# Kernel tuning notes

Measured on AMD Instinct MI355X. Metric: run time of the kernel, lower is better.

Reference implementation:

```python
import jax, jax.numpy as jnp
import numpy as np

B, T, I, H = 32, 512, 128, 512


def setup_inputs() -> dict:
    key = jax.random.key(0)
    ks = jax.random.split(key, 9)
    sH = 1.0 / np.sqrt(H)
    sI = 1.0 / np.sqrt(I)
    return {
        "values": jax.random.normal(ks[0], (B, T, I), jnp.float32),
        "Deltas": jax.random.uniform(ks[1], (B, T, 1), jnp.float32),
        "ys": jax.random.normal(ks[2], (B, T, 1), jnp.float32),
        # LSTMCell params (torch gate order: i, f, g, o)
        "W_ih": jax.random.uniform(ks[3], (4 * H, I), jnp.float32, -sH, sH),
        "W_hh": jax.random.uniform(ks[4], (4 * H, H), jnp.float32, -sH, sH),
        "b_ih": jax.random.uniform(ks[5], (4 * H,), jnp.float32, -sH, sH),
        "b_hh": jax.random.uniform(ks[6], (4 * H,), jnp.float32, -sH, sH),
        # atten_linear: input_size -> input_size
        "atten_W": jax.random.uniform(ks[7], (I, I), jnp.float32, -sI, sI),
        "atten_b": jax.random.uniform(ks[8], (I,), jnp.float32, -sI, sI),
    }


def lstm_cell(x, h, c, W_ih, W_hh, b_ih, b_hh):
    gates = x @ W_ih.T + b_ih + h @ W_hh.T + b_hh
    i, f, g, o = jnp.split(gates, 4, axis=-1)
    c_new = jax.nn.sigmoid(f) * c + jax.nn.sigmoid(i) * jnp.tanh(g)
    h_new = jax.nn.sigmoid(o) * jnp.tanh(c_new)
    return h_new, c_new


def reference(values, Deltas, ys, W_ih, W_hh, b_ih, b_hh, atten_W, atten_b):
    Bs, Ts, Is = values.shape
    Hs = W_hh.shape[1]
    dt = values.dtype
    # cumulative time gaps and pairwise decay matrix D[b,t,j] = cum[t] - cum[j]
    dcum = jnp.cumsum(Deltas, axis=-2)[..., 0]          # [B,T]
    D = dcum[:, :, None] - dcum[:, None, :]             # [B,T,T]
    # attention scores: linear(values) @ original_values^T
    v = values @ atten_W.T + atten_b                    # [B,T,I]
    a_tj = jnp.einsum('bti,bsi->bts', v, values)        # [B,T,T]
    # t = 0 step with zero initial state
    h0 = jnp.zeros((Bs, Hs), dt)
    c0 = jnp.zeros((Bs, Hs), dt)
    h, c = lstm_cell(v[:, 0], h0, c0, W_ih, W_hh, b_ih, b_hh)
    c_n = jnp.zeros((Bs, Ts, Hs), dt).at[:, 0].set(c)
    idx = jnp.arange(Ts)
    NEG = jnp.finfo(dt).min
    e = jnp.asarray(np.e, dt)

    def step(carry, t):
        h, c_n = carry
        mask = idx < t                                   # causal window j < t
        logits = jnp.where(mask, a_tj[:, t], NEG)
        alpha = jax.nn.softmax(logits, axis=-1)          # masked entries ~0
        w = jnp.where(mask, 1.0 / jnp.log(e + D[:, t]), 0.0)
        alpha = alpha * w
        C = jnp.einsum('bj,bjh->bh', alpha, c_n)         # weighted cell history
        h_new, c_new = lstm_cell(v[:, t], h, C, W_ih, W_hh, b_ih, b_hh)
        return (h_new, c_n.at[:, t].set(c_new)), h_new

    (_, _), hs = jax.lax.scan(step, (h, c_n), jnp.arange(1, Ts))
    h_n = jnp.concatenate([h[:, None], jnp.swapaxes(hs, 0, 1)], axis=1)
    return h_n
```

## Files before the change

kernel.cpp:

```cpp
#include <hip/hip_runtime.h>
#include <math.h>

#define B_  32
#define T_  512
#define I_  128
#define H_  512
#define G4_ 2048
#define GB_ 64
#define NG_ 4

__global__ __launch_bounds__(256) void gemm_abt(
    const float* __restrict__ A, const float* __restrict__ Bm, float* __restrict__ C,
    const float* __restrict__ bias, long sA, long sB, long sC, int ldc)
{
  __shared__ float Al[64][65];
  __shared__ float Bl[64][65];
  const long z = blockIdx.z;
  A += z * sA; Bm += z * sB; C += z * sC;
  const int m0 = blockIdx.x * 64, n0 = blockIdx.y * 64;
  const int tid = threadIdx.x;
  const int tx = tid & 15, ty = tid >> 4;
  float acc[4][4] = {};

  for (int h = 0; h < 2; ++h) {
    const int k0 = h * 64;
    __syncthreads();
    #pragma unroll
    for (int s = 0; s < 4; ++s) {
      int idx = tid + s * 256;
      int m  = idx >> 4;
      int k4 = (idx & 15) << 2;
      float4 a4 = *(const float4*)&A[(long)(m0 + m) * 128 + k0 + k4];
      Al[k4 + 0][m] = a4.x; Al[k4 + 1][m] = a4.y; Al[k4 + 2][m] = a4.z; Al[k4 + 3][m] = a4.w;
      float4 b4 = *(const float4*)&Bm[(long)(n0 + m) * 128 + k0 + k4];
      Bl[k4 + 0][m] = b4.x; Bl[k4 + 1][m] = b4.y; Bl[k4 + 2][m] = b4.z; Bl[k4 + 3][m] = b4.w;
    }
    __syncthreads();
    #pragma unroll 8
    for (int k = 0; k < 64; ++k) {
      float a0 = Al[k][ty*4+0], a1 = Al[k][ty*4+1], a2 = Al[k][ty*4+2], a3 = Al[k][ty*4+3];
      float b0 = Bl[k][tx*4+0], b1 = Bl[k][tx*4+1], b2 = Bl[k][tx*4+2], b3 = Bl[k][tx*4+3];
      acc[0][0] += a0*b0; acc[0][1] += a0*b1; acc[0][2] += a0*b2; acc[0][3] += a0*b3;
      acc[1][0] += a1*b0; acc[1][1] += a1*b1; acc[1][2] += a1*b2; acc[1][3] += a1*b3;
      acc[2][0] += a2*b0; acc[2][1] += a2*b1; acc[2][2] += a2*b2; acc[2][3] += a2*b3;
      acc[3][0] += a3*b0; acc[3][1] += a3*b1; acc[3][2] += a3*b2; acc[3][3] += a3*b3;
    }
  }
  #pragma unroll
  for (int i = 0; i < 4; ++i) {
    #pragma unroll
    for (int j = 0; j < 4; ++j) {
      float bb = bias ? bias[n0 + tx*4 + j] : 0.f;
      C[(long)(m0 + ty*4 + i) * ldc + n0 + tx*4 + j] = acc[i][j] + bb;
    }
  }
}

__global__ __launch_bounds__(512) void cumsum_k(const float* __restrict__ Deltas,
                                                float* __restrict__ dcum)
{
  __shared__ float s[512];
  const int b = blockIdx.x, t = threadIdx.x;
  s[t] = Deltas[b * 512 + t];
  __syncthreads();
  for (int off = 1; off < 512; off <<= 1) {
    float v = (t >= off) ? s[t - off] : 0.f;
    __syncthreads();
    s[t] += v;
    __syncthreads();
  }
  dcum[b * 512 + t] = s[t];
}

__global__ __launch_bounds__(64) void softmax_k(float* __restrict__ a,
                                                const float* __restrict__ dcum)
{
  const int t = blockIdx.x, b = blockIdx.y;
  float* row = a + ((long)b * T_ + t) * T_;
  const int lane = threadIdx.x;
  if (t == 0) {
    #pragma unroll
    for (int i = 0; i < 8; ++i) row[i * 64 + lane] = 0.f;
    return;
  }
  float vals[8];
  float mx = -3.4e38f;
  #pragma unroll
  for (int i = 0; i < 8; ++i) {
    int j = i * 64 + lane;
    float v = (j < t) ? row[j] : -3.4e38f;
    vals[i] = v; mx = fmaxf(mx, v);
  }
  #pragma unroll
  for (int off = 1; off < 64; off <<= 1) mx = fmaxf(mx, __shfl_xor(mx, off));
  float sum = 0.f;
  #pragma unroll
  for (int i = 0; i < 8; ++i) {
    int j = i * 64 + lane;
    float e = (j < t) ? expf(vals[i] - mx) : 0.f;
    vals[i] = e; sum += e;
  }
  #pragma unroll
  for (int off = 1; off < 64; off <<= 1) sum += __shfl_xor(sum, off);
  const float E = 2.718281828459045f;
  const float dct = dcum[b * 512 + t];
  const float inv = 1.f / sum;
  #pragma unroll
  for (int i = 0; i < 8; ++i) {
    int j = i * 64 + lane;
    float w = (j < t) ? 1.f / logf(E + dct - dcum[b * 512 + j]) : 0.f;
    row[j] = vals[i] * inv * w;
  }
}

__device__ __forceinline__ void st_wt(float* p, float v) {
  __hip_atomic_store(p, v, __ATOMIC_RELAXED, __HIP_MEMORY_SCOPE_AGENT);
}
__device__ __forceinline__ float ld_wt(const float* p) {
  return __hip_atomic_load(p, __ATOMIC_RELAXED, __HIP_MEMORY_SCOPE_AGENT);
}

__device__ __forceinline__ void bar_arrive(unsigned* cnt, unsigned* gen) {
  unsigned old = __hip_atomic_fetch_add(cnt, 1u, __ATOMIC_RELAXED, __HIP_MEMORY_SCOPE_AGENT);
  if (old == GB_ - 1u) {
    __hip_atomic_store(cnt, 0u, __ATOMIC_RELAXED, __HIP_MEMORY_SCOPE_AGENT);
    asm volatile("s_waitcnt vmcnt(0)" ::: "memory");
    __hip_atomic_fetch_add(gen, 1u, __ATOMIC_RELAXED, __HIP_MEMORY_SCOPE_AGENT);
  }
}
__device__ __forceinline__ int bar_wait(unsigned* gen, unsigned target, unsigned* abrt) {
  long spins = 0;
  for (;;) {
    unsigned g = __hip_atomic_load(gen, __ATOMIC_RELAXED, __HIP_MEMORY_SCOPE_AGENT);
    if ((int)(g - target) >= 0) return 0;
    if (((++spins) & 255) == 0) {
      if (__hip_atomic_load(abrt, __ATOMIC_RELAXED, __HIP_MEMORY_SCOPE_AGENT)) return 1;
      if (spins > 6000000L) {
        __hip_atomic_store(abrt, 1u, __ATOMIC_RELAXED, __HIP_MEMORY_SCOPE_AGENT);
        return 1;
      }
    }
    __builtin_amdgcn_s_sleep(1);
  }
}

__global__ __launch_bounds__(256, 1) void recurrent_k(
    const float* __restrict__ v_buf,
    const float* __restrict__ alpha,
    const float* __restrict__ W_ih,
    const float* __restrict__ W_hh,
    const float* __restrict__ b_ih, const float* __restrict__ b_hh,
    float* gates,
    float* out,
    unsigned* bar)
{
  extern __shared__ float lds[];
  float* hv  = lds;
  float* cn  = lds + 8 * 640;
  float* red = cn + 512 * 64;
  __shared__ int s_ab;

  const int tid = threadIdx.x;
  const int g = blockIdx.x;
  const int grp = g >> 6;
  const int rs = g & 63, bg = grp;
  const int b_u = g >> 3, hs = g & 7;
  const int r_l = tid >> 3, cg = tid & 7;
  const int row = rs * 32 + r_l;
  const int jg = tid >> 6, l = tid & 63;

  unsigned* cntA = bar + grp * 128 + 0;
  unsigned* genA = bar + grp * 128 + 32;
  unsigned* cntB = bar + grp * 128 + 64;
  unsigned* genB = bar + grp * 128 + 96;
  unsigned* abrt = bar + 1023;

  float4 wreg[20];
  #pragma unroll
  for (int k = 0; k < 20; ++k) {
    int c0 = cg * 4 + k * 32;
    if (k < 4) wreg[k] = *(const float4*)&W_ih[(long)row * I_ + c0];
    else       wreg[k] = *(const float4*)&W_hh[(long)row * H_ + (c0 - 128)];
  }
  const float bias = b_ih[row] + b_hh[row];

  for (int t = 0; t < T_; ++t) {
    if (tid == 0) s_ab = bar_wait(genA, (unsigned)t, abrt);
    __syncthreads();
    if (s_ab) return;

    {
      int bp = tid >> 5, c4 = (tid & 31) << 2;
      float4 vv = *(const float4*)&v_buf[((long)(bg * 8 + bp) * T_ + t) * I_ + c4];
      *(float4*)&hv[bp * 640 + c4] = vv;
    }
    if (t > 0) {
      #pragma unroll
      for (int s = 0; s < 16; ++s) {
        int idx = tid + s * 256;
        int bp = idx >> 9, c = idx & 511;
        hv[bp * 640 + 128 + c] = ld_wt(&out[((long)(bg * 8 + bp) * T_ + (t - 1)) * H_ + c]);
      }
    } else {
      #pragma unroll
      for (int s = 0; s < 16; ++s) {
        int idx = tid + s * 256;
        int bp = idx >> 9, c = idx & 511;
        hv[bp * 640 + 128 + c] = 0.f;
      }
    }
    __syncthreads();

    float acc[8] = {};
    #pragma unroll
    for (int k = 0; k < 20; ++k) {
      float4 w4 = wreg[k];
      #pragma unroll
      for (int bp = 0; bp < 8; ++bp) {
        float4 x = *(const float4*)&hv[bp * 640 + cg * 4 + k * 32];
        acc[bp] += w4.x * x.x + w4.y * x.y + w4.z * x.z + w4.w * x.w;
      }
    }
    #pragma unroll
    for (int off = 1; off < 8; off <<= 1) {
      #pragma unroll
      for (int bp = 0; bp < 8; ++bp) acc[bp] += __shfl_xor(acc[bp], off);
    }
    if (cg == 0) {
      #pragma unroll
      for (int bp = 0; bp < 8; ++bp)
        st_wt(&gates[(long)(bg * 8 + bp) * G4_ + row], acc[bp] + bias);
    }
    __syncthreads();
    if (tid == 0) bar_arrive(cntB, genB);

    float partial = 0.f;
    {
      const float* arow = alpha + ((long)b_u * T_ + t) * T_;
      int j0 = jg * 128, j1 = j0 + 128; if (j1 > t) j1 = t;
      for (int j = j0; j < j1; ++j)
        partial += arow[j] * cn[j * 64 + l];
    }
    red[tid] = partial;
    if (tid == 0) s_ab = bar_wait(genB, (unsigned)(t + 1), abrt);
    __syncthreads();
    if (s_ab) return;

    if (tid < 64) {
      const long gb = (long)b_u * G4_ + hs * 64 + l;
      float gi = ld_wt(&gates[gb]);
      float gf = ld_wt(&gates[gb + H_]);
      float gg = ld_wt(&gates[gb + 2 * H_]);
      float go = ld_wt(&gates[gb + 3 * H_]);
      float C  = red[l] + red[64 + l] + red[128 + l] + red[192 + l];
      float si = 1.f / (1.f + expf(-gi));
      float sf = 1.f / (1.f + expf(-gf));
      float so = 1.f / (1.f + expf(-go));
      float cnew = sf * C + si * tanhf(gg);
      float hnew = so * tanhf(cnew);
      st_wt(&out[((long)b_u * T_ + t) * H_ + hs * 64 + l], hnew);
      cn[t * 64 + l] = cnew;
    }
    __syncthreads();
    if (tid == 0) bar_arrive(cntA, genA);
  }
}

extern "C" void kernel_launch(void* const* d_in, const int* in_sizes, int n_in,
                              void* d_out, int out_size, void* d_ws, size_t ws_size,
                              hipStream_t stream)
{
  const float* values  = (const float*)d_in[0];
  const float* Deltas  = (const float*)d_in[1];
  const float* W_ih    = (const float*)d_in[3];
  const float* W_hh    = (const float*)d_in[4];
  const float* b_ih    = (const float*)d_in[5];
  const float* b_hh    = (const float*)d_in[6];
  const float* atten_W = (const float*)d_in[7];
  const float* atten_b = (const float*)d_in[8];
  float* out = (float*)d_out;

  char* ws = (char*)d_ws;
  unsigned* bar = (unsigned*)ws;
  float* v_buf  = (float*)(ws + 4096);
  float* a_buf  = (float*)(ws + 4096 + 8388608);
  float* dcum   = (float*)(ws + 4096 + 8388608 + 33554432);
  float* gates  = (float*)(ws + 4096 + 8388608 + 33554432 + 65536);

  hipMemsetAsync(bar, 0, 4096, stream);

  gemm_abt<<<dim3(256, 2, 1), 256, 0, stream>>>(values, atten_W, v_buf, atten_b,
                                                0, 0, 0, 128);
  cumsum_k<<<32, 512, 0, stream>>>(Deltas, dcum);
  gemm_abt<<<dim3(8, 8, 32), 256, 0, stream>>>(v_buf, values, a_buf, nullptr,
                                               512L * 128, 512L * 128, 512L * 512, 512);
  softmax_k<<<dim3(512, 32), 64, 0, stream>>>(a_buf, dcum);

  (void)hipFuncSetAttribute((const void*)recurrent_k,
                            hipFuncAttributeMaxDynamicSharedMemorySize, 152576);
  recurrent_k<<<256, 256, 152576, stream>>>(v_buf, a_buf, W_ih, W_hh, b_ih, b_hh,
                                            gates, out, bar);
}
```

Before: 16.60 ms.

## Replace counter barriers with per-block flags and precompute input projection off critical path

Swaps the atomic counter plus generation grid barrier for per-block monotonic flags. Each block publishes its step, and 64 lanes poll one group's flags together with a wave-wide all-check. This removes the serialized atomic increment chain from each barrier. The W_ih·v input projection for the next step is now computed while waiting on the second barrier, so it leaves the critical path, and the t=0 hidden-state zero-fill is skipped. The risks are more polling traffic and a lower spin timeout.

```diff
diff --git a/kernel.cpp b/kernel.cpp
--- a/kernel.cpp
+++ b/kernel.cpp
@@ -7,7 +7,6 @@
 #define H_  512
 #define G4_ 2048
 #define GB_ 64
-#define NG_ 4
 
 __global__ __launch_bounds__(256) void gemm_abt(
     const float* __restrict__ A, const float* __restrict__ Bm, float* __restrict__ C,
@@ -119,23 +118,19 @@
 __device__ __forceinline__ float ld_wt(const float* p) {
   return __hip_atomic_load(p, __ATOMIC_RELAXED, __HIP_MEMORY_SCOPE_AGENT);
 }
-
-__device__ __forceinline__ void bar_arrive(unsigned* cnt, unsigned* gen) {
-  unsigned old = __hip_atomic_fetch_add(cnt, 1u, __ATOMIC_RELAXED, __HIP_MEMORY_SCOPE_AGENT);
-  if (old == GB_ - 1u) {
-    __hip_atomic_store(cnt, 0u, __ATOMIC_RELAXED, __HIP_MEMORY_SCOPE_AGENT);
-    asm volatile("s_waitcnt vmcnt(0)" ::: "memory");
-    __hip_atomic_fetch_add(gen, 1u, __ATOMIC_RELAXED, __HIP_MEMORY_SCOPE_AGENT);
-  }
-}
-__device__ __forceinline__ int bar_wait(unsigned* gen, unsigned target, unsigned* abrt) {
+__device__ __forceinline__ void flag_set(unsigned* f, unsigned v) {
+  __hip_atomic_store(f, v, __ATOMIC_RELAXED, __HIP_MEMORY_SCOPE_AGENT);
+}
+__device__ __forceinline__ int poll64(const unsigned* flags, unsigned target,
+                                      unsigned* abrt) {
   long spins = 0;
   for (;;) {
-    unsigned g = __hip_atomic_load(gen, __ATOMIC_RELAXED, __HIP_MEMORY_SCOPE_AGENT);
-    if ((int)(g - target) >= 0) return 0;
-    if (((++spins) & 255) == 0) {
+    unsigned f = __hip_atomic_load(&flags[threadIdx.x], __ATOMIC_RELAXED,
+                                   __HIP_MEMORY_SCOPE_AGENT);
+    if (__all((int)(f >= target))) return 0;
+    if (((++spins) & 63) == 0) {
       if (__hip_atomic_load(abrt, __ATOMIC_RELAXED, __HIP_MEMORY_SCOPE_AGENT)) return 1;
-      if (spins > 6000000L) {
+      if (spins > 1500000L) {
         __hip_atomic_store(abrt, 1u, __ATOMIC_RELAXED, __HIP_MEMORY_SCOPE_AGENT);
         return 1;
       }
@@ -156,69 +151,75 @@
 {
   extern __shared__ float lds[];
   float* hv  = lds;
-  float* cn  = lds + 8 * 640;
+  float* cn  = lds + 8 * 512;
   float* red = cn + 512 * 64;
   __shared__ int s_ab;
 
   const int tid = threadIdx.x;
   const int g = blockIdx.x;
   const int grp = g >> 6;
-  const int rs = g & 63, bg = grp;
+  const int bg = grp;
+  const int rs = g & 63;
   const int b_u = g >> 3, hs = g & 7;
   const int r_l = tid >> 3, cg = tid & 7;
   const int row = rs * 32 + r_l;
   const int jg = tid >> 6, l = tid & 63;
 
-  unsigned* cntA = bar + grp * 128 + 0;
-  unsigned* genA = bar + grp * 128 + 32;
-  unsigned* cntB = bar + grp * 128 + 64;
-  unsigned* genB = bar + grp * 128 + 96;
-  unsigned* abrt = bar + 1023;
-
-  float4 wreg[20];
-  #pragma unroll
-  for (int k = 0; k < 20; ++k) {
-    int c0 = cg * 4 + k * 32;
-    if (k < 4) wreg[k] = *(const float4*)&W_ih[(long)row * I_ + c0];
-    else       wreg[k] = *(const float4*)&W_hh[(long)row * H_ + (c0 - 128)];
-  }
+  unsigned* flagA = bar;
+  unsigned* flagB = bar + 256;
+  unsigned* abrt  = bar + 512;
+  const unsigned* fA = flagA + grp * 64;
+  const unsigned* fB = flagB + grp * 64;
+
+  float4 wh[16];
+  #pragma unroll
+  for (int k = 0; k < 16; ++k)
+    wh[k] = *(const float4*)&W_hh[(long)row * H_ + cg * 4 + k * 32];
+  float4 wv[4];
+  #pragma unroll
+  for (int k = 0; k < 4; ++k)
+    wv[k] = *(const float4*)&W_ih[(long)row * I_ + cg * 4 + k * 32];
   const float bias = b_ih[row] + b_hh[row];
 
+  float vacc[8];
+  #pragma unroll
+  for (int bp = 0; bp < 8; ++bp) {
+    float a = 0.f;
+    #pragma unroll
+    for (int k = 0; k < 4; ++k) {
+      float4 x = *(const float4*)&v_buf[((long)(bg * 8 + bp) * T_) * I_ + cg * 4 + k * 32];
+      a += wv[k].x * x.x + wv[k].y * x.y + wv[k].z * x.z + wv[k].w * x.w;
+    }
+    vacc[bp] = a;
+  }
+
   for (int t = 0; t < T_; ++t) {
-    if (tid == 0) s_ab = bar_wait(genA, (unsigned)t, abrt);
+    if (tid < 64) { int ab = poll64(fA, (unsigned)t, abrt); if (tid == 0) s_ab = ab; }
     __syncthreads();
     if (s_ab) return;
 
-    {
-      int bp = tid >> 5, c4 = (tid & 31) << 2;
-      float4 vv = *(const float4*)&v_buf[((long)(bg * 8 + bp) * T_ + t) * I_ + c4];
-      *(float4*)&hv[bp * 640 + c4] = vv;
-    }
     if (t > 0) {
       #pragma unroll
       for (int s = 0; s < 16; ++s) {
         int idx = tid + s * 256;
         int bp = idx >> 9, c = idx & 511;
-        hv[bp * 640 + 128 + c] = ld_wt(&out[((long)(bg * 8 + bp) * T_ + (t - 1)) * H_ + c]);
+        hv[bp * 512 + c] = ld_wt(&out[((long)(bg * 8 + bp) * T_ + (t - 1)) * H_ + c]);
       }
-    } else {
-      #pragma unroll
-      for (int s = 0; s < 16; ++s) {
-        int idx = tid + s * 256;
-        int bp = idx >> 9, c = idx & 511;
-        hv[bp * 640 + 128 + c] = 0.f;
-      }
-    }
-    __syncthreads();
-
-    float acc[8] = {};
-    #pragma unroll
-    for (int k = 0; k < 20; ++k) {
-      float4 w4 = wreg[k];
-      #pragma unroll
-      for (int bp = 0; bp < 8; ++bp) {
-        float4 x = *(const float4*)&hv[bp * 640 + cg * 4 + k * 32];
-        acc[bp] += w4.x * x.x + w4.y * x.y + w4.z * x.z + w4.w * x.w;
+      __syncthreads();
+    }
+
+    float acc[8];
+    #pragma unroll
+    for (int bp = 0; bp < 8; ++bp) acc[bp] = vacc[bp];
+    if (t > 0) {
+      #pragma unroll
+      for (int k = 0; k < 16; ++k) {
+        float4 w4 = wh[k];
+        #pragma unroll
+        for (int bp = 0; bp < 8; ++bp) {
+          float4 x = *(const float4*)&hv[bp * 512 + cg * 4 + k * 32];
+          acc[bp] += w4.x * x.x + w4.y * x.y + w4.z * x.z + w4.w * x.w;
+        }
       }
     }
     #pragma unroll
@@ -232,8 +233,20 @@
         st_wt(&gates[(long)(bg * 8 + bp) * G4_ + row], acc[bp] + bias);
     }
     __syncthreads();
-    if (tid == 0) bar_arrive(cntB, genB);
-
+    if (tid == 0) flag_set(&flagB[g], (unsigned)(t + 1));
+
+    if (t + 1 < T_) {
+      #pragma unroll
+      for (int bp = 0; bp < 8; ++bp) {
+        float a = 0.f;
+        #pragma unroll
+        for (int k = 0; k < 4; ++k) {
+          float4 x = *(const float4*)&v_buf[((long)(bg * 8 + bp) * T_ + (t + 1)) * I_ + cg * 4 + k * 32];
+          a += wv[k].x * x.x + wv[k].y * x.y + wv[k].z * x.z + wv[k].w * x.w;
+        }
+        vacc[bp] = a;
+      }
+    }
     float partial = 0.f;
     {
       const float* arow = alpha + ((long)b_u * T_ + t) * T_;
@@ -242,7 +255,8 @@
         partial += arow[j] * cn[j * 64 + l];
     }
     red[tid] = partial;
-    if (tid == 0) s_ab = bar_wait(genB, (unsigned)(t + 1), abrt);
+
+    if (tid < 64) { int ab = poll64(fB, (unsigned)(t + 1), abrt); if (tid == 0) s_ab = ab; }
     __syncthreads();
     if (s_ab) return;
 
@@ -262,7 +276,7 @@
       cn[t * 64 + l] = cnew;
     }
     __syncthreads();
-    if (tid == 0) bar_arrive(cntA, genA);
+    if (tid == 0) flag_set(&flagA[g], (unsigned)(t + 1));
   }
 }
 
@@ -297,7 +311,7 @@
   softmax_k<<<dim3(512, 32), 64, 0, stream>>>(a_buf, dcum);
 
   (void)hipFuncSetAttribute((const void*)recurrent_k,
-                            hipFuncAttributeMaxDynamicSharedMemorySize, 152576);
-  recurrent_k<<<256, 256, 152576, stream>>>(v_buf, a_buf, W_ih, W_hh, b_ih, b_hh,
+                            hipFuncAttributeMaxDynamicSharedMemorySize, 148480);
+  recurrent_k<<<256, 256, 148480, stream>>>(v_buf, a_buf, W_ih, W_hh, b_ih, b_hh,
                                             gates, out, bar);
 }
```

Result: slower. 17.18 ms (+3.5%).
